# Kernel tuning notes

Hardware: AMD Instinct MI355X
Metric: run time of the kernel (lower is better)

## Reference

```python
import jax, jax.numpy as jnp
import numpy as np

B, N, IN_C, OUT_C, H, M, E = 1, 20000, 256, 64, 4, 30, 320000
EPS = 1e-6


def _projection_matrix(m, d, seed=0):
    # NodeFormer create_projection_matrix: stacked transposed-QR blocks, rows
    # rescaled by norms of iid gaussian rows (scaling=0).
    rng = np.random.RandomState(seed)
    blocks = []
    nb_full = m // d
    for _ in range(nb_full):
        q, _ = np.linalg.qr(rng.randn(d, d))
        blocks.append(q.T)
    rem = m - nb_full * d
    if rem > 0:
        q, _ = np.linalg.qr(rng.randn(d, d))
        blocks.append(q.T[:rem])
    final = np.vstack(blocks)
    multiplier = np.linalg.norm(rng.randn(m, d), axis=1)
    return jnp.asarray(multiplier[:, None] * final, dtype=jnp.float32)


def _linear(key, out_f, in_f):
    k1, k2 = jax.random.split(key)
    s = 1.0 / np.sqrt(in_f)
    w = jax.random.uniform(k1, (out_f, in_f), jnp.float32, -s, s)
    b = jax.random.uniform(k2, (out_f,), jnp.float32, -s, s)
    return w, b


def setup_inputs() -> dict:
    key = jax.random.key(0)
    ks = jax.random.split(key, 8)
    Wq_w, Wq_b = _linear(ks[3], H * OUT_C, IN_C)
    Wk_w, Wk_b = _linear(ks[4], H * OUT_C, IN_C)
    Wv_w, Wv_b = _linear(ks[5], H * OUT_C, IN_C)
    Wo_w, Wo_b = _linear(ks[6], OUT_C, H * OUT_C)
    return {
        'z': jax.random.normal(ks[0], (B, N, IN_C), jnp.float32),
        'feat': jax.random.normal(ks[1], (B, N, IN_C), jnp.float32),
        'edge_index': jax.random.randint(ks[2], (2, E), 0, N),
        'tau': jnp.asarray(0.25, jnp.float32),
        'Wq_w': Wq_w, 'Wq_b': Wq_b,
        'Wk_w': Wk_w, 'Wk_b': Wk_b,
        'Wv_w': Wv_w, 'Wv_b': Wv_b,
        'Wo_w': Wo_w, 'Wo_b': Wo_b,
        'b_param': jnp.full((1, H), 0.1, jnp.float32),  # rb_order=1, sigmoid init
        'proj': _projection_matrix(M, OUT_C),
    }


def _softmax_kernel(x, proj, is_query):
    # Performer positive softmax kernel feature map. x: [B,N,H,D] -> [B,N,H,M]
    d = x.shape[-1]
    x = x * (float(d) ** -0.25)
    ratio = 1.0 / jnp.sqrt(jnp.asarray(proj.shape[0], x.dtype))
    xd = jnp.einsum('bnhd,md->bnhm', x, proj)
    diag = 0.5 * jnp.sum(x * x, axis=-1, keepdims=True)
    if is_query:
        mx = jnp.max(xd, axis=-1, keepdims=True)
    else:
        mx = jnp.max(jnp.max(xd, axis=-1, keepdims=True), axis=1, keepdims=True)
    return ratio * (jnp.exp(xd - diag - mx) + EPS)


def reference(z, feat, edge_index, tau, Wq_w, Wq_b, Wk_w, Wk_b, Wv_w, Wv_b,
              Wo_w, Wo_b, b_param, proj):
    Bn, Nn = z.shape[0], z.shape[1]
    q = (feat @ Wq_w.T + Wq_b).reshape(Bn, Nn, H, OUT_C)
    k = (feat @ Wk_w.T + Wk_b).reshape(Bn, Nn, H, OUT_C)
    v = (z @ Wv_w.T + Wv_b).reshape(Bn, Nn, H, OUT_C)

    inv = 1.0 / jnp.sqrt(tau)
    qp = _softmax_kernel(q * inv, proj, True)    # [B,N,H,M]
    kp = _softmax_kernel(k * inv, proj, False)   # [B,N,H,M]

    # Linear (kernelized) attention, O(N*H*M*D)
    kvs = jnp.einsum('bnhm,bnhd->bhmd', kp, v)
    num = jnp.einsum('bnhm,bhmd->bnhd', qp, kvs)
    den = jnp.einsum('bnhm,bhm->bnh', qp, jnp.sum(kp, axis=1))[..., None]
    z_next = num / den                            # [B,N,H,D]

    # Relational bias: GCN-style normalized scatter with per-head scalar weight
    row, col = edge_index[0], edge_index[1]
    d_in = jnp.zeros((Nn,), z.dtype).at[col].add(1.0)
    d_out = jnp.zeros((Nn,), z.dtype).at[row].add(1.0)
    edge_w = jnp.nan_to_num(jnp.sqrt(1.0 / d_in[col]) * jnp.sqrt(1.0 / d_out[row]),
                            nan=0.0, posinf=0.0, neginf=0.0)    # [E]
    msgs = v[:, row] * edge_w[None, :, None, None]              # [B,E,H,D]
    agg = jnp.zeros_like(v).at[:, col].add(msgs)                # [B,N,H,D]
    z_next = z_next + jax.nn.sigmoid(b_param[0])[None, None, :, None] * agg

    out = z_next.reshape(Bn, Nn, H * OUT_C) @ Wo_w.T + Wo_b     # [B,N,OUT_C]
    return out
```

## Files before the change

kernel.cpp:

```cpp
#include <hip/hip_runtime.h>

#define NN 20000
#define EE 320000
#define RATIO_F 0.18257418583505536f
#define EPS_F 1e-6f
#define SCALE_D4 0.35355339059327373f
#define NCH 157

typedef _Float16 f16x8 __attribute__((ext_vector_type(8)));
typedef _Float16 f16x4 __attribute__((ext_vector_type(4)));
typedef float f32x4 __attribute__((ext_vector_type(4)));

__device__ __forceinline__ unsigned fenc(float x) {
  unsigned u = __float_as_uint(x);
  return (u & 0x80000000u) ? ~u : (u | 0x80000000u);
}
__device__ __forceinline__ float fdec(unsigned u) {
  return (u & 0x80000000u) ? __uint_as_float(u & 0x7FFFFFFFu) : __uint_as_float(~u);
}
__device__ __forceinline__ void fma4(float* a, float s, float4 b) {
  a[0] = fmaf(s, b.x, a[0]);
  a[1] = fmaf(s, b.y, a[1]);
  a[2] = fmaf(s, b.z, a[2]);
  a[3] = fmaf(s, b.w, a[3]);
}
__device__ __forceinline__ void gload16(const void* g, void* l) {
  __builtin_amdgcn_global_load_lds(
      (const __attribute__((address_space(1))) unsigned int*)g,
      (__attribute__((address_space(3))) unsigned int*)l, 16, 0, 0);
}

__global__ __launch_bounds__(256)
void k0_build(const float* __restrict__ Wq, const float* __restrict__ Wk,
              const float* __restrict__ Wv, const float* __restrict__ bq,
              const float* __restrict__ bk, const float* __restrict__ bv,
              const float* __restrict__ proj, const float* __restrict__ tau,
              const float* __restrict__ Wo, const int* __restrict__ ei,
              const float* __restrict__ feat, const float* __restrict__ zin,
              _Float16* __restrict__ Wf, float* __restrict__ bbig,
              _Float16* __restrict__ WoFh, _Float16* __restrict__ WoFl,
              int* __restrict__ dini, int* __restrict__ douti,
              _Float16* __restrict__ feath, _Float16* __restrict__ zh16) {
  const int blk = blockIdx.x;
  const int i = threadIdx.x;
  if (blk >= 1401) {
    int cb = blk - 1401;
    const float* src;
    _Float16* dst;
    if (cb < 2500) { src = feat; dst = feath; }
    else           { src = zin;  dst = zh16; cb -= 2500; }
    const size_t off = (size_t)cb * 2048 + i * 8;
    const float4 a = *(const float4*)(src + off);
    const float4 b = *(const float4*)(src + off + 4);
    f16x8 o;
    o[0] = (_Float16)a.x; o[1] = (_Float16)a.y;
    o[2] = (_Float16)a.z; o[3] = (_Float16)a.w;
    o[4] = (_Float16)b.x; o[5] = (_Float16)b.y;
    o[6] = (_Float16)b.z; o[7] = (_Float16)b.w;
    *(f16x8*)(dst + off) = o;
    return;
  }
  if (blk >= 1088) {
    const int q = (blk - 1088) * 256 + i;
    if (q < EE / 4) {
      const int4 r4 = *(const int4*)(ei + q * 4);
      const int4 c4 = *(const int4*)(ei + EE + q * 4);
      atomicAdd(&dini[c4.x], 1); atomicAdd(&dini[c4.y], 1);
      atomicAdd(&dini[c4.z], 1); atomicAdd(&dini[c4.w], 1);
      atomicAdd(&douti[r4.x], 1); atomicAdd(&douti[r4.y], 1);
      atomicAdd(&douti[r4.z], 1); atomicAdd(&douti[r4.w], 1);
    }
    return;
  }
  const int kt = i >> 5, gg = (i >> 3) & 3, j = i & 7;
  if (blk >= 1024) {
    const int col = blk - 1024;
    const float val = Wo[col * 256 + i];
    const int lane = gg * 16 + (col & 15);
    const size_t off = (size_t)((col >> 4) * 8 + kt) * 512 + lane * 8 + j;
    const _Float16 hb = (_Float16)val;
    WoFh[off] = hb;
    WoFl[off] = (_Float16)(val - (float)hb);
    return;
  }
  const int col = blk;
  const float s = rsqrtf(tau[0]) * SCALE_D4;
  float val = 0.f, bias = 0.f;
  if (col < 256) {
    val = Wq[col * 256 + i]; bias = bq[col];
  } else if (col < 512) {
    const int c = col - 256;
    val = Wk[c * 256 + i]; bias = bk[c];
  } else if (col < 768) {
    const int c = col - 512;
    val = Wv[c * 256 + i]; bias = bv[c];
  } else {
    const int rr = col - 768;
    const int grp = rr >> 7;
    const int h = (rr >> 5) & 3, m = rr & 31;
    if (m < 30) {
      const float* W = grp ? Wk : Wq;
      const float* bb = grp ? bk : bq;
      float a = 0.f, ba = 0.f;
#pragma unroll 8
      for (int d = 0; d < 64; ++d) {
        const float pr = proj[m * 64 + d];
        a  = fmaf(pr, W[(h * 64 + d) * 256 + i], a);
        ba = fmaf(pr, bb[h * 64 + d], ba);
      }
      val = s * a; bias = s * ba;
    }
  }
  const int lane = gg * 16 + (col & 15);
  const size_t off = (size_t)((col >> 4) * 8 + kt) * 512 + lane * 8 + j;
  Wf[off] = (_Float16)val;
  if (i == 0) bbig[col] = bias;
}

__device__ __forceinline__ int ct_of(int s, int isv, int h, int y) {
  if (isv) return 32 + (y - 4) * 8 + s;
  if (s < 4)  return h * 4 + s;
  if (s < 8)  return 16 + h * 4 + (s - 4);
  if (s < 10) return 48 + 2 * h + (s - 8);
  return 56 + 2 * h + (s - 10);
}

__global__ __launch_bounds__(512, 4)
void k1m(const _Float16* __restrict__ feath, const _Float16* __restrict__ zh16,
         const _Float16* __restrict__ Wf, const float* __restrict__ bbig,
         const float* __restrict__ tau,
         _Float16* __restrict__ qph, _Float16* __restrict__ kbufh,
         _Float16* __restrict__ vh, unsigned* __restrict__ kmaxU,
         const int* __restrict__ ei, const int* __restrict__ coff,
         int* __restrict__ cursor, int2* __restrict__ crowR,
         const int* __restrict__ douti) {
  __shared__ __align__(16) _Float16 blds[12 * 2048];
  const int blk = blockIdx.x;
  const int t = threadIdx.x;
  if (blk >= 942) {
    const int e = (blk - 942) * 512 + t;
    const int r = ei[e], c = ei[EE + e];
    const float w = rsqrtf((float)douti[r]);
    const int pos = atomicAdd(&cursor[c], 1);
    int2 rec; rec.x = r; rec.y = __float_as_int(w);
    crowR[coff[c] + pos] = rec;
    return;
  }
  const int y = blk / 157;
  const int h = y & 3;
  const int wid = t >> 6, lane = t & 63;
  const int g = lane >> 4, cl = lane & 15;
  const int rbase = (blk - y * 157) * 128 + wid * 16;
  int arow = rbase + cl; if (arow > NN - 1) arow = NN - 1;

  if (y < 4) {
    const _Float16* arp = feath + (size_t)arow * 256;
#pragma unroll
    for (int r = 0; r < 6; ++r) {
      const int idx = r * 4096 + t * 8;
      const int s = idx >> 11, wi = idx & 2047;
      gload16(Wf + (size_t)ct_of(s, 0, h, y) * 4096 + wi, &blds[idx]);
    }
    f16x8 Ah[4];
#pragma unroll
    for (int l = 0; l < 4; ++l)
      Ah[l] = *(const f16x8*)(arp + l * 32 + g * 8);
    __syncthreads();
    f16x8 Ah2[4];
#pragma unroll
    for (int l = 0; l < 4; ++l)
      Ah2[l] = *(const f16x8*)(arp + (l + 4) * 32 + g * 8);
    f32x4 acc[12];
#pragma unroll
    for (int s = 0; s < 12; ++s) acc[s] = (f32x4){0.f, 0.f, 0.f, 0.f};
#pragma unroll
    for (int ktl = 0; ktl < 4; ++ktl) {
#pragma unroll
      for (int s = 0; s < 12; ++s) {
        const f16x8 b = *(const f16x8*)&blds[s * 2048 + ktl * 512 + lane * 8];
        acc[s] = __builtin_amdgcn_mfma_f32_16x16x32_f16(Ah[ktl], b, acc[s], 0, 0, 0);
      }
    }
    __syncthreads();
#pragma unroll
    for (int r = 0; r < 6; ++r) {
      const int idx = r * 4096 + t * 8;
      const int s = idx >> 11, wi = idx & 2047;
      gload16(Wf + (size_t)ct_of(s, 0, h, y) * 4096 + 2048 + wi, &blds[idx]);
    }
    __syncthreads();
#pragma unroll
    for (int ktl = 0; ktl < 4; ++ktl) {
#pragma unroll
      for (int s = 0; s < 12; ++s) {
        const f16x8 b = *(const f16x8*)&blds[s * 2048 + ktl * 512 + lane * 8];
        acc[s] = __builtin_amdgcn_mfma_f32_16x16x32_f16(Ah2[ktl], b, acc[s], 0, 0, 0);
      }
    }
#pragma unroll
    for (int s = 0; s < 12; ++s) {
      const float bb = bbig[ct_of(s, 0, h, y) * 16 + cl];
#pragma unroll
      for (int j = 0; j < 4; ++j) acc[s][j] += bb;
    }
    const float sc = rsqrtf(tau[0]) * SCALE_D4;
    const float h2 = 0.5f * sc * sc;
    float dsq[4], dsk[4];
#pragma unroll
    for (int j = 0; j < 4; ++j) {
      dsq[j] = acc[0][j] * acc[0][j] + acc[1][j] * acc[1][j] +
               acc[2][j] * acc[2][j] + acc[3][j] * acc[3][j];
      dsk[j] = acc[4][j] * acc[4][j] + acc[5][j] * acc[5][j] +
               acc[6][j] * acc[6][j] + acc[7][j] * acc[7][j];
    }
#pragma unroll
    for (int m = 1; m < 16; m <<= 1) {
#pragma unroll
      for (int j = 0; j < 4; ++j) {
        dsq[j] += __shfl_xor(dsq[j], m);
        dsk[j] += __shfl_xor(dsk[j], m);
      }
    }
    {
#pragma unroll
      for (int j = 0; j < 4; ++j) {
        const float x0 = acc[8][j], x1 = acc[9][j];
        float mv = fmaxf(x0, (cl < 14) ? x1 : -3.4e38f);
#pragma unroll
        for (int m = 1; m < 16; m <<= 1) mv = fmaxf(mv, __shfl_xor(mv, m));
        const float dg = h2 * dsq[j];
        const int r = rbase + 4 * g + j;
        if (r < NN) {
          _Float16* dst = qph + (size_t)r * 120 + h * 30;
          dst[cl] = (_Float16)(RATIO_F * (expf(x0 - dg - mv) + EPS_F));
          if (cl < 14)
            dst[16 + cl] = (_Float16)(RATIO_F * (expf(x1 - dg - mv) + EPS_F));
        }
      }
    }
    {
      float wmax = -3.4e38f;
#pragma unroll
      for (int j = 0; j < 4; ++j) {
        const float x0 = acc[10][j], x1 = acc[11][j];
        float mv = fmaxf(x0, (cl < 14) ? x1 : -3.4e38f);
#pragma unroll
        for (int m = 1; m < 16; m <<= 1) mv = fmaxf(mv, __shfl_xor(mv, m));
        wmax = fmaxf(wmax, mv);
        const float dg = h2 * dsk[j];
        const int r = rbase + 4 * g + j;
        if (r < NN) {
          _Float16* dst = kbufh + (size_t)r * 120 + h * 30;
          dst[cl] = (_Float16)(x0 - dg);
          if (cl < 14) dst[16 + cl] = (_Float16)(x1 - dg);
        }
      }
      wmax = fmaxf(wmax, __shfl_xor(wmax, 16));
      wmax = fmaxf(wmax, __shfl_xor(wmax, 32));
      if (lane == 0) atomicMax(&kmaxU[h], fenc(wmax));
    }
  } else {
    const _Float16* arp = zh16 + (size_t)arow * 256;
#pragma unroll
    for (int r = 0; r < 4; ++r) {
      const int idx = r * 4096 + t * 8;
      const int s = idx >> 11, wi = idx & 2047;
      gload16(Wf + (size_t)ct_of(s, 1, h, y) * 4096 + wi, &blds[idx]);
    }
    f16x8 Ah[4];
#pragma unroll
    for (int l = 0; l < 4; ++l)
      Ah[l] = *(const f16x8*)(arp + l * 32 + g * 8);
    __syncthreads();
    f16x8 Ah2[4];
#pragma unroll
    for (int l = 0; l < 4; ++l)
      Ah2[l] = *(const f16x8*)(arp + (l + 4) * 32 + g * 8);
    f32x4 acc[8];
#pragma unroll
    for (int s = 0; s < 8; ++s) acc[s] = (f32x4){0.f, 0.f, 0.f, 0.f};
#pragma unroll
    for (int ktl = 0; ktl < 4; ++ktl) {
#pragma unroll
      for (int s = 0; s < 8; ++s) {
        const f16x8 b = *(const f16x8*)&blds[s * 2048 + ktl * 512 + lane * 8];
        acc[s] = __builtin_amdgcn_mfma_f32_16x16x32_f16(Ah[ktl], b, acc[s], 0, 0, 0);
      }
    }
    __syncthreads();
#pragma unroll
    for (int r = 0; r < 4; ++r) {
      const int idx = r * 4096 + t * 8;
      const int s = idx >> 11, wi = idx & 2047;
      gload16(Wf + (size_t)ct_of(s, 1, h, y) * 4096 + 2048 + wi, &blds[idx]);
    }
    __syncthreads();
#pragma unroll
    for (int ktl = 0; ktl < 4; ++ktl) {
#pragma unroll
      for (int s = 0; s < 8; ++s) {
        const f16x8 b = *(const f16x8*)&blds[s * 2048 + ktl * 512 + lane * 8];
        acc[s] = __builtin_amdgcn_mfma_f32_16x16x32_f16(Ah2[ktl], b, acc[s], 0, 0, 0);
      }
    }
#pragma unroll
    for (int s = 0; s < 8; ++s) {
      const int ct = ct_of(s, 1, h, y);
      const float bb = bbig[ct * 16 + cl];
      const int colb = (ct - 32) * 16 + cl;
#pragma unroll
      for (int j = 0; j < 4; ++j) {
        const int r = rbase + 4 * g + j;
        if (r < NN) vh[(size_t)r * 256 + colb] = (_Float16)(acc[s][j] + bb);
      }
    }
  }
}

__global__ __launch_bounds__(256)
void k3_kvs(const _Float16* __restrict__ kbr, const _Float16* __restrict__ vh,
            const unsigned* __restrict__ kmaxU, float* __restrict__ partial) {
  __shared__ float kpch[128 * 32];
  __shared__ float vch[128 * 68];
  const int h = blockIdx.y;
  const int n0 = blockIdx.x * 128;
  const int cnt = min(128, NN - n0);
  const int t = threadIdx.x;
  const float mx = fdec(kmaxU[h]);
  const int m = t >> 3, dg = t & 7, d0 = dg * 8;
#pragma unroll
  for (int l = 0; l < 15; ++l) {
    const int flat = l * 256 + t;
    const int nl = flat / 30, mm = flat - nl * 30;
    kpch[nl * 32 + mm] = (nl < cnt)
        ? RATIO_F * (expf((float)kbr[(size_t)(n0 + nl) * 120 + h * 30 + mm] - mx) + EPS_F)
        : 0.f;
  }
#pragma unroll
  for (int l = 0; l < 8; ++l) {
    const int f4 = l * 256 + t;
    const int nl = f4 >> 4, dd = (f4 & 15) * 4;
    float4 vv = make_float4(0.f, 0.f, 0.f, 0.f);
    if (nl < cnt) {
      f16x4 u = *(const f16x4*)(vh + (size_t)(n0 + nl) * 256 + h * 64 + dd);
      vv = make_float4((float)u[0], (float)u[1], (float)u[2], (float)u[3]);
    }
    *(float4*)&vch[nl * 68 + dd] = vv;
  }
  __syncthreads();
  float acc[8] = {0, 0, 0, 0, 0, 0, 0, 0};
  float asum = 0.f;
  const int ms = (m < 30) ? m : 0;
  for (int nl = 0; nl < cnt; ++nl) {
    const float kv = kpch[nl * 32 + ms];
    const float4 va = *(const float4*)&vch[nl * 68 + d0];
    const float4 vb = *(const float4*)&vch[nl * 68 + d0 + 4];
    fma4(&acc[0], kv, va);
    fma4(&acc[4], kv, vb);
    asum += kv;
  }
  if (m < 30) {
    float* dst = partial + ((size_t)blockIdx.y * NCH + blockIdx.x) * 1952 + m * 64 + d0;
#pragma unroll
    for (int j = 0; j < 8; ++j) dst[j] = acc[j];
    if (dg == 0)
      partial[((size_t)blockIdx.y * NCH + blockIdx.x) * 1952 + 1920 + m] = asum;
  }
}

__global__ __launch_bounds__(256)
void k7g3b(const int* __restrict__ coff, const int2* __restrict__ crowR,
           const _Float16* __restrict__ vh, _Float16* __restrict__ aggh,
           const float* __restrict__ partial, float* __restrict__ kvs,
           float* __restrict__ ksum) {
  const int blk = blockIdx.x;
  if (blk >= 5000) {
    const int idx = (blk - 5000) * 256 + threadIdx.x;
    if (idx >= 4 * 1952) return;
    const int h = idx / 1952, q = idx - h * 1952;
    float s = 0.f;
    for (int c = 0; c < NCH; ++c)
      s += partial[((size_t)h * NCH + c) * 1952 + q];
    if (q < 1920) kvs[h * 1920 + q] = s;
    else if (q < 1950) ksum[h * 30 + (q - 1920)] = s;
    return;
  }
  const int node = blk * 4 + (threadIdx.x >> 6);
  const int lane = threadIdx.x & 63;
  const int o0 = coff[node], o1 = coff[node + 1];
  float a0 = 0.f, a1 = 0.f, a2 = 0.f, a3 = 0.f;
  if (o1 > o0) {
    int e = o0;
    for (; e + 16 <= o1; e += 16) {
      int2 rc[16];
#pragma unroll
      for (int u = 0; u < 16; ++u) rc[u] = crowR[e + u];
#pragma unroll
      for (int u = 0; u < 16; ++u) {
        const float w = __int_as_float(rc[u].y);
        const f16x4 vv = *(const f16x4*)(vh + (size_t)rc[u].x * 256 + lane * 4);
        a0 = fmaf(w, (float)vv[0], a0);
        a1 = fmaf(w, (float)vv[1], a1);
        a2 = fmaf(w, (float)vv[2], a2);
        a3 = fmaf(w, (float)vv[3], a3);
      }
    }
    for (; e + 4 <= o1; e += 4) {
      int2 rc[4];
#pragma unroll
      for (int u = 0; u < 4; ++u) rc[u] = crowR[e + u];
#pragma unroll
      for (int u = 0; u < 4; ++u) {
        const float w = __int_as_float(rc[u].y);
        const f16x4 vv = *(const f16x4*)(vh + (size_t)rc[u].x * 256 + lane * 4);
        a0 = fmaf(w, (float)vv[0], a0);
        a1 = fmaf(w, (float)vv[1], a1);
        a2 = fmaf(w, (float)vv[2], a2);
        a3 = fmaf(w, (float)vv[3], a3);
      }
    }
    for (; e < o1; ++e) {
      const int2 rc = crowR[e];
      const float w = __int_as_float(rc.y);
      const f16x4 vv = *(const f16x4*)(vh + (size_t)rc.x * 256 + lane * 4);
      a0 = fmaf(w, (float)vv[0], a0);
      a1 = fmaf(w, (float)vv[1], a1);
      a2 = fmaf(w, (float)vv[2], a2);
      a3 = fmaf(w, (float)vv[3], a3);
    }
    const float rin = rsqrtf((float)(o1 - o0));
    a0 *= rin; a1 *= rin; a2 *= rin; a3 *= rin;
  }
  f16x4 st;
  st[0] = (_Float16)a0; st[1] = (_Float16)a1;
  st[2] = (_Float16)a2; st[3] = (_Float16)a3;
  *(f16x4*)(aggh + (size_t)node * 256 + lane * 4) = st;
}

__global__ __launch_bounds__(256)
void k4_attn(const _Float16* __restrict__ qph, const float* __restrict__ kvs,
             const float* __restrict__ ksum, const _Float16* __restrict__ aggh,
             const float* __restrict__ bp, _Float16* __restrict__ zh) {
  __shared__ float kvsl[120 * 68];
  __shared__ float ksl[120];
  __shared__ float qpl[32 * 120];
  const int t = threadIdx.x;
  const int n0 = blockIdx.x * 32;
#pragma unroll
  for (int l = 0; l < 30; ++l) {
    const int f = l * 256 + t;
    const int hm = f >> 6, d = f & 63;
    kvsl[hm * 68 + d] = kvs[f];
  }
  if (t < 120) ksl[t] = ksum[t];
#pragma unroll
  for (int l = 0; l < 15; ++l) {
    const int f = l * 256 + t;
    qpl[f] = (float)qph[(size_t)n0 * 120 + f];
  }
  __syncthreads();
  const int nl = t >> 3, dg = t & 7, d0 = dg * 8;
  const float* qrow = &qpl[nl * 120];
  float den[4] = {0, 0, 0, 0};
  for (int m = 0; m < 30; ++m) {
#pragma unroll
    for (int hh = 0; hh < 4; ++hh) den[hh] = fmaf(qrow[hh * 30 + m], ksl[hh * 30 + m], den[hh]);
  }
  float acc[4][8] = {};
  for (int m = 0; m < 30; ++m) {
#pragma unroll
    for (int hh = 0; hh < 4; ++hh) {
      const float qv = qrow[hh * 30 + m];
      const float* kr = &kvsl[(hh * 30 + m) * 68 + d0];
      const float4 ka = *(const float4*)kr;
      const float4 kb = *(const float4*)(kr + 4);
      fma4(&acc[hh][0], qv, ka);
      fma4(&acc[hh][4], qv, kb);
    }
  }
  const size_t n = n0 + nl;
#pragma unroll
  for (int hh = 0; hh < 4; ++hh) {
    const float inv = 1.0f / den[hh];
    const float sg = 1.f / (1.f + expf(-bp[hh]));
    const f16x8 ag = *(const f16x8*)(aggh + n * 256 + hh * 64 + d0);
    f16x8 o;
#pragma unroll
    for (int jj = 0; jj < 8; ++jj)
      o[jj] = (_Float16)(acc[hh][jj] * inv + sg * (float)ag[jj]);
    *(f16x8*)(zh + n * 256 + hh * 64 + d0) = o;
  }
}

__global__ __launch_bounds__(1024)
void k6a_scan(const int* __restrict__ cnt, int* __restrict__ off) {
  __shared__ int s[1024];
  const int t = threadIdx.x;
  int4 v[5];
  int sum = 0;
  const int4* p4 = (const int4*)(cnt + t * 20);
#pragma unroll
  for (int i = 0; i < 5; ++i) {
    v[i] = p4[i];
    sum += v[i].x + v[i].y + v[i].z + v[i].w;
  }
  s[t] = sum;
  __syncthreads();
  for (int o = 1; o < 1024; o <<= 1) {
    const int add = (t >= o) ? s[t - o] : 0;
    __syncthreads();
    s[t] += add;
    __syncthreads();
  }
  int run = (t == 0) ? 0 : s[t - 1];
  if (t == 0) off[0] = 0;
  const int base = t * 20;
#pragma unroll
  for (int i = 0; i < 5; ++i) {
    const int vals[4] = {v[i].x, v[i].y, v[i].z, v[i].w};
#pragma unroll
    for (int j = 0; j < 4; ++j) {
      const int idx = base + i * 4 + j;
      if (idx < NN) { run += vals[j]; off[idx + 1] = run; }
    }
  }
}

__global__ __launch_bounds__(512, 4)
void k8m_out(const _Float16* __restrict__ zh, const _Float16* __restrict__ WoFh,
             const _Float16* __restrict__ WoFl, const float* __restrict__ bo,
             float* __restrict__ out) {
  __shared__ __align__(16) _Float16 blds[8 * 4096];
  const int t = threadIdx.x;
  const int wid = t >> 6, lane = t & 63;
  const int g = lane >> 4, cl = lane & 15;
  const int rt = wid >> 2, ct = wid & 3;
  const int rbase = blockIdx.x * 32 + rt * 16;
  int arow = rbase + cl; if (arow > NN - 1) arow = NN - 1;
#pragma unroll
  for (int s = 0; s < 4; ++s) {
    gload16(WoFh + (size_t)s * 4096 + t * 8, &blds[(s * 512 + t) * 8]);
    gload16(WoFl + (size_t)s * 4096 + t * 8, &blds[((s + 4) * 512 + t) * 8]);
  }
  const _Float16* zr = zh + (size_t)arow * 256;
  f16x8 Ah[8];
#pragma unroll
  for (int kt = 0; kt < 8; ++kt)
    Ah[kt] = *(const f16x8*)(zr + kt * 32 + g * 8);
  __syncthreads();
  f32x4 acc = {0.f, 0.f, 0.f, 0.f};
#pragma unroll
  for (int kt = 0; kt < 8; ++kt) {
    const f16x8 bh = *(const f16x8*)&blds[ct * 4096 + kt * 512 + lane * 8];
    const f16x8 bl = *(const f16x8*)&blds[(ct + 4) * 4096 + kt * 512 + lane * 8];
    acc = __builtin_amdgcn_mfma_f32_16x16x32_f16(Ah[kt], bh, acc, 0, 0, 0);
    acc = __builtin_amdgcn_mfma_f32_16x16x32_f16(Ah[kt], bl, acc, 0, 0, 0);
  }
  const float bb = bo[ct * 16 + cl];
#pragma unroll
  for (int j = 0; j < 4; ++j) {
    const int r = rbase + 4 * g + j;
    if (r < NN) out[(size_t)r * 64 + ct * 16 + cl] = acc[j] + bb;
  }
}

extern "C" void kernel_launch(void* const* d_in, const int* in_sizes, int n_in,
                              void* d_out, int out_size, void* d_ws, size_t ws_size,
                              hipStream_t stream) {
  (void)in_sizes; (void)n_in; (void)out_size; (void)ws_size;
  const float* z    = (const float*)d_in[0];
  const float* feat = (const float*)d_in[1];
  const int*   ei   = (const int*)d_in[2];
  const float* tau  = (const float*)d_in[3];
  const float* Wq_w = (const float*)d_in[4];
  const float* Wq_b = (const float*)d_in[5];
  const float* Wk_w = (const float*)d_in[6];
  const float* Wk_b = (const float*)d_in[7];
  const float* Wv_w = (const float*)d_in[8];
  const float* Wv_b = (const float*)d_in[9];
  const float* Wo_w = (const float*)d_in[10];
  const float* Wo_b = (const float*)d_in[11];
  const float* bp   = (const float*)d_in[12];
  const float* proj = (const float*)d_in[13];
  float* out = (float*)d_out;

  char* p = (char*)d_ws;
  auto alloc = [&](size_t bytes) { char* r = p; p += (bytes + 255) & ~(size_t)255; return r; };
  _Float16* Wf    = (_Float16*)alloc((size_t)256 * 1024 * 2);
  _Float16* WoFh  = (_Float16*)alloc((size_t)64 * 256 * 2);
  _Float16* WoFl  = (_Float16*)alloc((size_t)64 * 256 * 2);
  float*    bbig  = (float*)alloc(1024 * 4);
  _Float16* feath = (_Float16*)alloc((size_t)NN * 256 * 2);
  _Float16* zh16  = (_Float16*)alloc((size_t)NN * 256 * 2);
  _Float16* vh    = (_Float16*)alloc((size_t)NN * 256 * 2);
  _Float16* aggh  = (_Float16*)alloc((size_t)NN * 256 * 2);
  _Float16* qph   = (_Float16*)alloc((size_t)NN * 120 * 2);
  _Float16* kbufh = (_Float16*)alloc((size_t)NN * 120 * 2);
  _Float16* zh    = (_Float16*)alloc((size_t)NN * 256 * 2);
  int2*     crowR = (int2*)alloc((size_t)EE * 8);
  int*      coff  = (int*)alloc((size_t)(NN + 1) * 4);
  float*    partial = (float*)alloc((size_t)4 * NCH * 1952 * 4);
  float*    kvs   = (float*)alloc(7680 * 4);
  float*    ksum  = (float*)alloc(120 * 4);
  char* z0 = p;
  unsigned* kmaxU = (unsigned*)alloc(16);
  int*      dini  = (int*)alloc((size_t)20480 * 4);
  int*      douti = (int*)alloc((size_t)NN * 4);
  int*      cursor= (int*)alloc((size_t)NN * 4);
  char* z1 = p;

  hipMemsetAsync(z0, 0, (size_t)(z1 - z0), stream);

  k0_build<<<1401 + 5000, 256, 0, stream>>>(
      Wq_w, Wk_w, Wv_w, Wq_b, Wk_b, Wv_b, proj, tau, Wo_w, ei, feat, z,
      Wf, bbig, WoFh, WoFl, dini, douti, feath, zh16);
  k6a_scan<<<1, 1024, 0, stream>>>(dini, coff);
  k1m<<<1567, 512, 0, stream>>>(feath, zh16, Wf, bbig, tau, qph, kbufh, vh,
                                kmaxU, ei, coff, cursor, crowR, douti);
  k3_kvs<<<dim3(NCH, 4), 256, 0, stream>>>(kbufh, vh, kmaxU, partial);
  k7g3b<<<5000 + (4 * 1952 + 255) / 256, 256, 0, stream>>>(
      coff, crowR, vh, aggh, partial, kvs, ksum);
  k4_attn<<<NN / 32, 256, 0, stream>>>(qph, kvs, ksum, aggh, bp, zh);
  k8m_out<<<628, 512, 0, stream>>>(zh, WoFh, WoFl, Wo_b, out);
}
```

Baseline: 233.0 us.

## Double-buffer weight tiles in LDS for projection GEMM kernel

Splits the K dimension of the fused Q/K/V projection into four quarter-chunks with a two-slot LDS buffer, so the next weight chunk is loaded while MFMAs run on the current one. All A-row fragments are loaded up front into registers. This is meant to hide global-to-LDS latency that the old two-phase load/sync/compute sequence exposed. It costs more barriers and higher register pressure from holding eight A fragments, which could reduce occupancy.

```diff
diff --git a/kernel.cpp b/kernel.cpp
--- a/kernel.cpp
+++ b/kernel.cpp
@@ -134,7 +134,7 @@
          const int* __restrict__ ei, const int* __restrict__ coff,
          int* __restrict__ cursor, int2* __restrict__ crowR,
          const int* __restrict__ douti) {
-  __shared__ __align__(16) _Float16 blds[12 * 2048];
+  __shared__ __align__(16) _Float16 blds[2][12 * 1024];
   const int blk = blockIdx.x;
   const int t = threadIdx.x;
   if (blk >= 942) {
@@ -155,48 +155,46 @@
 
   if (y < 4) {
     const _Float16* arp = feath + (size_t)arow * 256;
-#pragma unroll
-    for (int r = 0; r < 6; ++r) {
+    f16x8 Ah[8];
+#pragma unroll
+    for (int l = 0; l < 8; ++l)
+      Ah[l] = *(const f16x8*)(arp + l * 32 + g * 8);
+#pragma unroll
+    for (int r = 0; r < 3; ++r) {
       const int idx = r * 4096 + t * 8;
-      const int s = idx >> 11, wi = idx & 2047;
-      gload16(Wf + (size_t)ct_of(s, 0, h, y) * 4096 + wi, &blds[idx]);
-    }
-    f16x8 Ah[4];
-#pragma unroll
-    for (int l = 0; l < 4; ++l)
-      Ah[l] = *(const f16x8*)(arp + l * 32 + g * 8);
+      const int s = idx >> 10, wi = idx & 1023;
+      gload16(Wf + (size_t)ct_of(s, 0, h, y) * 4096 + wi, &blds[0][idx]);
+    }
     __syncthreads();
-    f16x8 Ah2[4];
-#pragma unroll
-    for (int l = 0; l < 4; ++l)
-      Ah2[l] = *(const f16x8*)(arp + (l + 4) * 32 + g * 8);
+
     f32x4 acc[12];
 #pragma unroll
     for (int s = 0; s < 12; ++s) acc[s] = (f32x4){0.f, 0.f, 0.f, 0.f};
-#pragma unroll
-    for (int ktl = 0; ktl < 4; ++ktl) {
-#pragma unroll
-      for (int s = 0; s < 12; ++s) {
-        const f16x8 b = *(const f16x8*)&blds[s * 2048 + ktl * 512 + lane * 8];
-        acc[s] = __builtin_amdgcn_mfma_f32_16x16x32_f16(Ah[ktl], b, acc[s], 0, 0, 0);
-      }
-    }
-    __syncthreads();
-#pragma unroll
-    for (int r = 0; r < 6; ++r) {
-      const int idx = r * 4096 + t * 8;
-      const int s = idx >> 11, wi = idx & 2047;
-      gload16(Wf + (size_t)ct_of(s, 0, h, y) * 4096 + 2048 + wi, &blds[idx]);
-    }
-    __syncthreads();
-#pragma unroll
-    for (int ktl = 0; ktl < 4; ++ktl) {
-#pragma unroll
-      for (int s = 0; s < 12; ++s) {
-        const f16x8 b = *(const f16x8*)&blds[s * 2048 + ktl * 512 + lane * 8];
-        acc[s] = __builtin_amdgcn_mfma_f32_16x16x32_f16(Ah2[ktl], b, acc[s], 0, 0, 0);
-      }
-    }
+
+#pragma unroll
+    for (int qi = 0; qi < 4; ++qi) {
+      const int buf = qi & 1;
+      if (qi < 3) {
+#pragma unroll
+        for (int r = 0; r < 3; ++r) {
+          const int idx = r * 4096 + t * 8;
+          const int s = idx >> 10, wi = idx & 1023;
+          gload16(Wf + (size_t)ct_of(s, 0, h, y) * 4096 + (qi + 1) * 1024 + wi,
+                  &blds[buf ^ 1][idx]);
+        }
+      }
+#pragma unroll
+      for (int ktl = 0; ktl < 2; ++ktl) {
+        const f16x8 a = Ah[qi * 2 + ktl];
+#pragma unroll
+        for (int s = 0; s < 12; ++s) {
+          const f16x8 b = *(const f16x8*)&blds[buf][s * 1024 + ktl * 512 + lane * 8];
+          acc[s] = __builtin_amdgcn_mfma_f32_16x16x32_f16(a, b, acc[s], 0, 0, 0);
+        }
+      }
+      __syncthreads();
+    }
+
 #pragma unroll
     for (int s = 0; s < 12; ++s) {
       const float bb = bbig[ct_of(s, 0, h, y) * 16 + cl];
@@ -261,48 +259,46 @@
     }
   } else {
     const _Float16* arp = zh16 + (size_t)arow * 256;
-#pragma unroll
-    for (int r = 0; r < 4; ++r) {
+    f16x8 Ah[8];
+#pragma unroll
+    for (int l = 0; l < 8; ++l)
+      Ah[l] = *(const f16x8*)(arp + l * 32 + g * 8);
+#pragma unroll
+    for (int r = 0; r < 2; ++r) {
       const int idx = r * 4096 + t * 8;
-      const int s = idx >> 11, wi = idx & 2047;
-      gload16(Wf + (size_t)ct_of(s, 1, h, y) * 4096 + wi, &blds[idx]);
-    }
-    f16x8 Ah[4];
-#pragma unroll
-    for (int l = 0; l < 4; ++l)
-      Ah[l] = *(const f16x8*)(arp + l * 32 + g * 8);
+      const int s = idx >> 10, wi = idx & 1023;
+      gload16(Wf + (size_t)ct_of(s, 1, h, y) * 4096 + wi, &blds[0][idx]);
+    }
     __syncthreads();
-    f16x8 Ah2[4];
-#pragma unroll
-    for (int l = 0; l < 4; ++l)
-      Ah2[l] = *(const f16x8*)(arp + (l + 4) * 32 + g * 8);
+
     f32x4 acc[8];
 #pragma unroll
     for (int s = 0; s < 8; ++s) acc[s] = (f32x4){0.f, 0.f, 0.f, 0.f};
-#pragma unroll
-    for (int ktl = 0; ktl < 4; ++ktl) {
-#pragma unroll
-      for (int s = 0; s < 8; ++s) {
-        const f16x8 b = *(const f16x8*)&blds[s * 2048 + ktl * 512 + lane * 8];
-        acc[s] = __builtin_amdgcn_mfma_f32_16x16x32_f16(Ah[ktl], b, acc[s], 0, 0, 0);
-      }
-    }
-    __syncthreads();
-#pragma unroll
-    for (int r = 0; r < 4; ++r) {
-      const int idx = r * 4096 + t * 8;
-      const int s = idx >> 11, wi = idx & 2047;
-      gload16(Wf + (size_t)ct_of(s, 1, h, y) * 4096 + 2048 + wi, &blds[idx]);
-    }
-    __syncthreads();
-#pragma unroll
-    for (int ktl = 0; ktl < 4; ++ktl) {
-#pragma unroll
-      for (int s = 0; s < 8; ++s) {
-        const f16x8 b = *(const f16x8*)&blds[s * 2048 + ktl * 512 + lane * 8];
-        acc[s] = __builtin_amdgcn_mfma_f32_16x16x32_f16(Ah2[ktl], b, acc[s], 0, 0, 0);
-      }
-    }
+
+#pragma unroll
+    for (int qi = 0; qi < 4; ++qi) {
+      const int buf = qi & 1;
+      if (qi < 3) {
+#pragma unroll
+        for (int r = 0; r < 2; ++r) {
+          const int idx = r * 4096 + t * 8;
+          const int s = idx >> 10, wi = idx & 1023;
+          gload16(Wf + (size_t)ct_of(s, 1, h, y) * 4096 + (qi + 1) * 1024 + wi,
+                  &blds[buf ^ 1][idx]);
+        }
+      }
+#pragma unroll
+      for (int ktl = 0; ktl < 2; ++ktl) {
+        const f16x8 a = Ah[qi * 2 + ktl];
+#pragma unroll
+        for (int s = 0; s < 8; ++s) {
+          const f16x8 b = *(const f16x8*)&blds[buf][s * 1024 + ktl * 512 + lane * 8];
+          acc[s] = __builtin_amdgcn_mfma_f32_16x16x32_f16(a, b, acc[s], 0, 0, 0);
+        }
+      }
+      __syncthreads();
+    }
+
 #pragma unroll
     for (int s = 0; s < 8; ++s) {
       const int ct = ct_of(s, 1, h, y);
```

Result: no change. 236.5 us (+1.5%).

## Fuse attention combine with output projection and drop fp16 split-weight correction

Applied to the files above, without the earlier changes.

Merges the attention-combine kernel and the output projection GEMM into one kernel. The fused z tile stays in shared memory as fp16 instead of round-tripping through global memory, which also removes one launch. The Wo weights move from a hi/lo fp16 split to a single fp16 copy, halving the MFMA count and weight loads at some cost in output precision. Shared memory is reused between the kvs/qp buffers and the weight tile, which raises LDS use per block.

```diff
diff --git a/kernel.cpp b/kernel.cpp
--- a/kernel.cpp
+++ b/kernel.cpp
@@ -38,7 +38,7 @@
               const float* __restrict__ Wo, const int* __restrict__ ei,
               const float* __restrict__ feat, const float* __restrict__ zin,
               _Float16* __restrict__ Wf, float* __restrict__ bbig,
-              _Float16* __restrict__ WoFh, _Float16* __restrict__ WoFl,
+              _Float16* __restrict__ WoFh,
               int* __restrict__ dini, int* __restrict__ douti,
               _Float16* __restrict__ feath, _Float16* __restrict__ zh16) {
   const int blk = blockIdx.x;
@@ -78,9 +78,7 @@
     const float val = Wo[col * 256 + i];
     const int lane = gg * 16 + (col & 15);
     const size_t off = (size_t)((col >> 4) * 8 + kt) * 512 + lane * 8 + j;
-    const _Float16 hb = (_Float16)val;
-    WoFh[off] = hb;
-    WoFl[off] = (_Float16)(val - (float)hb);
+    WoFh[off] = (_Float16)val;
     return;
   }
   const int col = blk;
@@ -438,12 +436,16 @@
 }
 
 __global__ __launch_bounds__(256)
-void k4_attn(const _Float16* __restrict__ qph, const float* __restrict__ kvs,
+void k48_out(const _Float16* __restrict__ qph, const float* __restrict__ kvs,
              const float* __restrict__ ksum, const _Float16* __restrict__ aggh,
-             const float* __restrict__ bp, _Float16* __restrict__ zh) {
-  __shared__ float kvsl[120 * 68];
+             const float* __restrict__ bp, const _Float16* __restrict__ WoFh,
+             const float* __restrict__ bo, float* __restrict__ out) {
+  __shared__ __align__(16) char smem[48000];
   __shared__ float ksl[120];
-  __shared__ float qpl[32 * 120];
+  __shared__ __align__(16) _Float16 zl[32 * 260];
+  float* kvsl = (float*)smem;
+  float* qpl  = (float*)(smem + 32640);
+  _Float16* wol = (_Float16*)smem;
   const int t = threadIdx.x;
   const int n0 = blockIdx.x * 32;
 #pragma unroll
@@ -459,36 +461,71 @@
     qpl[f] = (float)qph[(size_t)n0 * 120 + f];
   }
   __syncthreads();
-  const int nl = t >> 3, dg = t & 7, d0 = dg * 8;
-  const float* qrow = &qpl[nl * 120];
-  float den[4] = {0, 0, 0, 0};
-  for (int m = 0; m < 30; ++m) {
-#pragma unroll
-    for (int hh = 0; hh < 4; ++hh) den[hh] = fmaf(qrow[hh * 30 + m], ksl[hh * 30 + m], den[hh]);
-  }
-  float acc[4][8] = {};
-  for (int m = 0; m < 30; ++m) {
+  {
+    const int nl = t >> 3, dg = t & 7, d0 = dg * 8;
+    const float* qrow = &qpl[nl * 120];
+    float den[4] = {0, 0, 0, 0};
+    for (int m = 0; m < 30; ++m) {
+#pragma unroll
+      for (int hh = 0; hh < 4; ++hh)
+        den[hh] = fmaf(qrow[hh * 30 + m], ksl[hh * 30 + m], den[hh]);
+    }
+    float acc[4][8] = {};
+    for (int m = 0; m < 30; ++m) {
+#pragma unroll
+      for (int hh = 0; hh < 4; ++hh) {
+        const float qv = qrow[hh * 30 + m];
+        const float* kr = &kvsl[(hh * 30 + m) * 68 + d0];
+        const float4 ka = *(const float4*)kr;
+        const float4 kb = *(const float4*)(kr + 4);
+        fma4(&acc[hh][0], qv, ka);
+        fma4(&acc[hh][4], qv, kb);
+      }
+    }
+    const size_t n = n0 + nl;
 #pragma unroll
     for (int hh = 0; hh < 4; ++hh) {
-      const float qv = qrow[hh * 30 + m];
-      const float* kr = &kvsl[(hh * 30 + m) * 68 + d0];
-      const float4 ka = *(const float4*)kr;
-      const float4 kb = *(const float4*)(kr + 4);
-      fma4(&acc[hh][0], qv, ka);
-      fma4(&acc[hh][4], qv, kb);
-    }
-  }
-  const size_t n = n0 + nl;
-#pragma unroll
-  for (int hh = 0; hh < 4; ++hh) {
-    const float inv = 1.0f / den[hh];
-    const float sg = 1.f / (1.f + expf(-bp[hh]));
-    const f16x8 ag = *(const f16x8*)(aggh + n * 256 + hh * 64 + d0);
-    f16x8 o;
-#pragma unroll
-    for (int jj = 0; jj < 8; ++jj)
-      o[jj] = (_Float16)(acc[hh][jj] * inv + sg * (float)ag[jj]);
-    *(f16x8*)(zh + n * 256 + hh * 64 + d0) = o;
+      const float inv = 1.0f / den[hh];
+      const float sg = 1.f / (1.f + expf(-bp[hh]));
+      const f16x8 ag = *(const f16x8*)(aggh + n * 256 + hh * 64 + d0);
+      f16x8 o;
+#pragma unroll
+      for (int jj = 0; jj < 8; ++jj)
+        o[jj] = (_Float16)(acc[hh][jj] * inv + sg * (float)ag[jj]);
+      *(f16x8*)&zl[nl * 260 + hh * 64 + d0] = o;
+    }
+  }
+  __syncthreads();
+#pragma unroll
+  for (int r = 0; r < 8; ++r) {
+    const int idx = r * 256 + t;
+    gload16(WoFh + (size_t)idx * 8, &wol[idx * 8]);
+  }
+  __syncthreads();
+  {
+    const int wid = t >> 6, lane = t & 63;
+    const int g = lane >> 4, cl = lane & 15;
+    const int rt = wid >> 1, ctp = (wid & 1) * 2;
+    f16x8 Ah[8];
+#pragma unroll
+    for (int kt = 0; kt < 8; ++kt)
+      Ah[kt] = *(const f16x8*)&zl[(rt * 16 + cl) * 260 + kt * 32 + g * 8];
+    f32x4 acc0 = {0.f, 0.f, 0.f, 0.f}, acc1 = {0.f, 0.f, 0.f, 0.f};
+#pragma unroll
+    for (int kt = 0; kt < 8; ++kt) {
+      const f16x8 b0 = *(const f16x8*)&wol[ctp * 4096 + kt * 512 + lane * 8];
+      const f16x8 b1 = *(const f16x8*)&wol[(ctp + 1) * 4096 + kt * 512 + lane * 8];
+      acc0 = __builtin_amdgcn_mfma_f32_16x16x32_f16(Ah[kt], b0, acc0, 0, 0, 0);
+      acc1 = __builtin_amdgcn_mfma_f32_16x16x32_f16(Ah[kt], b1, acc1, 0, 0, 0);
+    }
+    const float bb0 = bo[ctp * 16 + cl];
+    const float bb1 = bo[(ctp + 1) * 16 + cl];
+#pragma unroll
+    for (int j = 0; j < 4; ++j) {
+      const int r = n0 + rt * 16 + 4 * g + j;
+      out[(size_t)r * 64 + ctp * 16 + cl] = acc0[j] + bb0;
+      out[(size_t)r * 64 + (ctp + 1) * 16 + cl] = acc1[j] + bb1;
+    }
   }
 }
 
@@ -523,44 +560,6 @@
       const int idx = base + i * 4 + j;
       if (idx < NN) { run += vals[j]; off[idx + 1] = run; }
     }
-  }
-}
-
-__global__ __launch_bounds__(512, 4)
-void k8m_out(const _Float16* __restrict__ zh, const _Float16* __restrict__ WoFh,
-             const _Float16* __restrict__ WoFl, const float* __restrict__ bo,
-             float* __restrict__ out) {
-  __shared__ __align__(16) _Float16 blds[8 * 4096];
-  const int t = threadIdx.x;
-  const int wid = t >> 6, lane = t & 63;
-  const int g = lane >> 4, cl = lane & 15;
-  const int rt = wid >> 2, ct = wid & 3;
-  const int rbase = blockIdx.x * 32 + rt * 16;
-  int arow = rbase + cl; if (arow > NN - 1) arow = NN - 1;
-#pragma unroll
-  for (int s = 0; s < 4; ++s) {
-    gload16(WoFh + (size_t)s * 4096 + t * 8, &blds[(s * 512 + t) * 8]);
-    gload16(WoFl + (size_t)s * 4096 + t * 8, &blds[((s + 4) * 512 + t) * 8]);
-  }
-  const _Float16* zr = zh + (size_t)arow * 256;
-  f16x8 Ah[8];
-#pragma unroll
-  for (int kt = 0; kt < 8; ++kt)
-    Ah[kt] = *(const f16x8*)(zr + kt * 32 + g * 8);
-  __syncthreads();
-  f32x4 acc = {0.f, 0.f, 0.f, 0.f};
-#pragma unroll
-  for (int kt = 0; kt < 8; ++kt) {
-    const f16x8 bh = *(const f16x8*)&blds[ct * 4096 + kt * 512 + lane * 8];
-    const f16x8 bl = *(const f16x8*)&blds[(ct + 4) * 4096 + kt * 512 + lane * 8];
-    acc = __builtin_amdgcn_mfma_f32_16x16x32_f16(Ah[kt], bh, acc, 0, 0, 0);
-    acc = __builtin_amdgcn_mfma_f32_16x16x32_f16(Ah[kt], bl, acc, 0, 0, 0);
-  }
-  const float bb = bo[ct * 16 + cl];
-#pragma unroll
-  for (int j = 0; j < 4; ++j) {
-    const int r = rbase + 4 * g + j;
-    if (r < NN) out[(size_t)r * 64 + ct * 16 + cl] = acc[j] + bb;
   }
 }
 
@@ -588,7 +587,6 @@
   auto alloc = [&](size_t bytes) { char* r = p; p += (bytes + 255) & ~(size_t)255; return r; };
   _Float16* Wf    = (_Float16*)alloc((size_t)256 * 1024 * 2);
   _Float16* WoFh  = (_Float16*)alloc((size_t)64 * 256 * 2);
-  _Float16* WoFl  = (_Float16*)alloc((size_t)64 * 256 * 2);
   float*    bbig  = (float*)alloc(1024 * 4);
   _Float16* feath = (_Float16*)alloc((size_t)NN * 256 * 2);
   _Float16* zh16  = (_Float16*)alloc((size_t)NN * 256 * 2);
@@ -596,7 +594,6 @@
   _Float16* aggh  = (_Float16*)alloc((size_t)NN * 256 * 2);
   _Float16* qph   = (_Float16*)alloc((size_t)NN * 120 * 2);
   _Float16* kbufh = (_Float16*)alloc((size_t)NN * 120 * 2);
-  _Float16* zh    = (_Float16*)alloc((size_t)NN * 256 * 2);
   int2*     crowR = (int2*)alloc((size_t)EE * 8);
   int*      coff  = (int*)alloc((size_t)(NN + 1) * 4);
   float*    partial = (float*)alloc((size_t)4 * NCH * 1952 * 4);
@@ -613,13 +610,12 @@
 
   k0_build<<<1401 + 5000, 256, 0, stream>>>(
       Wq_w, Wk_w, Wv_w, Wq_b, Wk_b, Wv_b, proj, tau, Wo_w, ei, feat, z,
-      Wf, bbig, WoFh, WoFl, dini, douti, feath, zh16);
+      Wf, bbig, WoFh, dini, douti, feath, zh16);
   k6a_scan<<<1, 1024, 0, stream>>>(dini, coff);
   k1m<<<1567, 512, 0, stream>>>(feath, zh16, Wf, bbig, tau, qph, kbufh, vh,
                                 kmaxU, ei, coff, cursor, crowR, douti);
   k3_kvs<<<dim3(NCH, 4), 256, 0, stream>>>(kbufh, vh, kmaxU, partial);
   k7g3b<<<5000 + (4 * 1952 + 255) / 256, 256, 0, stream>>>(
       coff, crowR, vh, aggh, partial, kvs, ksum);
-  k4_attn<<<NN / 32, 256, 0, stream>>>(qph, kvs, ksum, aggh, bp, zh);
-  k8m_out<<<628, 512, 0, stream>>>(zh, WoFh, WoFl, Wo_b, out);
-}
+  k48_out<<<NN / 32, 256, 0, stream>>>(qph, kvs, ksum, aggh, bp, WoFh, Wo_b, out);
+}
```

Result: no change. 229.0 us (-1.7%).
